# Performance work log

Measured on AMD Instinct MI355X. Metric: run time of the kernel, lower is better.

## Reference

```python
import jax, jax.numpy as jnp
import numpy as np

N_NODES = 50000
N_EDGES = 800000
D_IN = 128
D_HID = 128
D_OUT = 128
N_LAYERS = 2
NEG_SLOPE = 0.2


def leaky(x):
    return jnp.where(x >= 0, x, NEG_SLOPE * x)


def setup_inputs() -> dict:
    key = jax.random.key(0)
    ks = jax.random.split(key, 12)
    s = 1.0 / np.sqrt(D_HID)
    feats = jax.random.normal(ks[0], (N_NODES, D_IN), dtype=jnp.float32)
    src = jax.random.randint(ks[1], (N_EDGES,), 0, N_NODES)
    dst = jax.random.randint(ks[2], (N_EDGES,), 0, N_NODES)
    # SIRConv params per layer: W_Q (dst), W_K (src), W_R (output proj)
    Wq = jax.random.normal(ks[3], (N_LAYERS, D_IN, D_HID), dtype=jnp.float32) * s
    bq = jnp.zeros((N_LAYERS, D_HID), dtype=jnp.float32)
    Wk = jax.random.normal(ks[4], (N_LAYERS, D_IN, D_HID), dtype=jnp.float32) * s
    bk = jnp.zeros((N_LAYERS, D_HID), dtype=jnp.float32)
    Wr = jax.random.normal(ks[5], (N_LAYERS, D_HID, D_HID), dtype=jnp.float32) * s
    br = jnp.zeros((N_LAYERS, D_HID), dtype=jnp.float32)
    # Jumping-knowledge readouts: one per entry of feats_list (input + each layer);
    # input_dim == hidden_dim so weights stack along the leading axis.
    Wro = jax.random.normal(ks[6], (N_LAYERS + 1, D_HID, D_OUT), dtype=jnp.float32) * s
    bro = jnp.zeros((N_LAYERS + 1, D_OUT), dtype=jnp.float32)
    return {"feats": feats, "Wq": Wq, "bq": bq, "Wk": Wk, "bk": bk,
            "Wr": Wr, "br": br, "Wro": Wro, "bro": bro,
            "src": src, "dst": dst}


def reference(feats, Wq, bq, Wk, bk, Wr, br, Wro, bro, src, dst):
    # mean-aggregation denominator: in-degree, clamped to 1
    deg = jax.ops.segment_sum(jnp.ones((N_EDGES,), jnp.float32), dst,
                              num_segments=N_NODES)
    denom = jnp.maximum(deg, 1.0)[:, None]  # [N, 1]

    feats_list = [feats]
    h = feats
    for i in range(N_LAYERS):
        hq = h @ Wq[i] + bq[i]          # [N, H] (dst transform)
        hk = h @ Wk[i] + bk[i]          # [N, H] (src transform)
        m = leaky(hq[dst] + hk[src])    # [E, H] contextualized messages
        agg = jax.ops.segment_sum(m, dst, num_segments=N_NODES) / denom
        h = agg @ Wr[i] + br[i]         # conv output (+ residual = 0)
        h = leaky(h)                    # norm='none', dropout=0
        feats_list.append(h)

    # jumping-knowledge readout: sum of per-stage linear readouts
    score = feats_list[0] @ Wro[0] + bro[0]
    for i in range(1, N_LAYERS + 1):
        score = score + feats_list[i] @ Wro[i] + bro[i]
    return score
```

## Files before the change

### kernel.cpp

```cpp
#include <hip/hip_runtime.h>

#define NN 50000
#define NE 800000
#define D 128
#define NEG 0.2f

#define NBLK1 256
#define TILE1 3125
#define NB2 196
#define CAP2 8192
#define NT64 782

#define SB_PREP 576
#define SB_CONV 6250
#define SB_HIST NBLK1
#define SB_TOTAL (SB_PREP + SB_CONV + SB_HIST)

typedef short bf8_t __attribute__((ext_vector_type(8)));
typedef float f4_t __attribute__((ext_vector_type(4)));

__device__ __forceinline__ unsigned short f2bf(float f) {
  unsigned int u = __float_as_uint(f);
  return (unsigned short)((u + 0x7FFF + ((u >> 16) & 1)) >> 16);
}
__device__ __forceinline__ float bf2f(unsigned int b) { return __uint_as_float(b << 16); }

__device__ __forceinline__ f4_t MF(bf8_t a, bf8_t b, f4_t c) {
  return __builtin_amdgcn_mfma_f32_16x16x32_bf16(a, b, c, 0, 0, 0);
}

__device__ __forceinline__ int swz_u(int u) { return u ^ ((u >> 4) & 7); }


__device__ __forceinline__ void stage_w(unsigned short* wbuf,
                                        const unsigned short* __restrict__ WT, int t) {
#pragma unroll
  for (int i = 0; i < 8; ++i) {
    int u = t + i * 256;
    *(uint4*)(wbuf + swz_u(u) * 8) = *(const uint4*)(WT + u * 8);
  }
}

__device__ __forceinline__ void load_a16(const unsigned short* __restrict__ A,
                                         int base, int l15, int quad, bf8_t (&afr)[4]) {
  int r = base + l15;
  if (r >= NN) r = NN - 1;
  const unsigned short* p = A + (size_t)r * D + quad * 8;
#pragma unroll
  for (int kc = 0; kc < 4; ++kc) afr[kc] = *(const bf8_t*)(p + kc * 32);
}

__device__ __forceinline__ void load_a16_lds(const unsigned short* buf, int wave,
                                             int l15, int quad, bf8_t (&afr)[4]) {
  const int r = wave * 16 + l15;
#pragma unroll
  for (int kc = 0; kc < 4; ++kc)
    afr[kc] = *(const bf8_t*)(buf + swz_u(r * 16 + kc * 4 + quad) * 8);
}

__device__ __forceinline__ void tile16(const unsigned short* wbuf, const bf8_t (&afr)[4],
                                       int l15, int quad, f4_t (&acc)[8]) {
#pragma unroll
  for (int kc = 0; kc < 4; ++kc)
#pragma unroll
    for (int nt = 0; nt < 8; ++nt) {
      bf8_t b = *(const bf8_t*)(wbuf + swz_u((nt * 16 + l15) * 16 + kc * 4 + quad) * 8);
      acc[nt] = MF(afr[kc], b, acc[nt]);
    }
}

__device__ __forceinline__ void store_c(unsigned short* __restrict__ C,
                                        const float* __restrict__ bias,
                                        const f4_t (&acc)[8], int base, int l15, int quad,
                                        bool lk) {
#pragma unroll
  for (int nt = 0; nt < 8; ++nt) {
    int col = nt * 16 + l15;
    float bb = bias[col];
#pragma unroll
    for (int reg = 0; reg < 4; ++reg) {
      int row = base + quad * 4 + reg;
      if (row < NN) {
        float v = acc[nt][reg] + bb;
        if (lk) v = v >= 0.f ? v : NEG * v;
        C[(size_t)row * D + col] = f2bf(v);
      }
    }
  }
}

__global__ __launch_bounds__(256) void setup(
    const float* __restrict__ Wq, const float* __restrict__ Wk,
    const float* __restrict__ Wr, const float* __restrict__ Wro,
    const float* __restrict__ feats, const int* __restrict__ dst,
    unsigned short* __restrict__ WT, unsigned short* __restrict__ x0,
    int* __restrict__ H) {
  __shared__ int cnt[NB2];
  const int b = blockIdx.x;
  const int t = threadIdx.x;
  if (b < SB_PREP) {
    const int m = b >> 6, xb = b & 63;
    const float* src;
    if (m < 2) src = Wq + m * D * D;
    else if (m < 4) src = Wk + (m - 2) * D * D;
    else if (m < 6) src = Wr + (m - 4) * D * D;
    else src = Wro + (m - 6) * D * D;
    const int n = xb * 2 + (t >> 7);
    const int k = t & 127;
    WT[(size_t)m * D * D + n * D + k] = f2bf(src[k * D + n]);
  } else if (b < SB_PREP + SB_CONV) {
    int i = ((b - SB_PREP) * 256 + t) * 4;
    float4 v = *(const float4*)(feats + i);
    ushort4 o = {f2bf(v.x), f2bf(v.y), f2bf(v.z), f2bf(v.w)};
    *(ushort4*)(x0 + i) = o;
  } else {
    const int blk = b - SB_PREP - SB_CONV;
    if (t < NB2) cnt[t] = 0;
    __syncthreads();
    const int beg = blk * TILE1, end = beg + TILE1;
    for (int i = beg + t; i < end; i += 256) atomicAdd(&cnt[dst[i] >> 8], 1);
    __syncthreads();
    if (t < NB2) H[t * NBLK1 + blk] = cnt[t];
  }
}

__global__ __launch_bounds__(256) void p1_scan(const int* __restrict__ H,
                                               int* __restrict__ gofs) {
  __shared__ int sd[256];
  __shared__ int wsum[4];
  const int bin = blockIdx.x;
  const int t = threadIdx.x;
  const int wave = t >> 6, lane = t & 63;
  int part = 0;
  for (int b2 = 0; b2 < bin; ++b2) part += H[b2 * NBLK1 + t];
  for (int off = 32; off; off >>= 1) part += __shfl_down(part, off, 64);
  if (lane == 0) wsum[wave] = part;
  __syncthreads();
  const int base = wsum[0] + wsum[1] + wsum[2] + wsum[3];
  int x = H[bin * NBLK1 + t];
  sd[t] = x;
  __syncthreads();
  int acc = x;
  for (int off = 1; off < 256; off <<= 1) {
    int y = (t >= off) ? sd[t - off] : 0;
    __syncthreads();
    acc += y;
    sd[t] = acc;
    __syncthreads();
  }
  gofs[bin * NBLK1 + t] = base + (acc - x);
}

__global__ __launch_bounds__(256) void p1_scatter(const int* __restrict__ src,
                                                  const int* __restrict__ dst,
                                                  const int* __restrict__ gofs,
                                                  unsigned int* __restrict__ ebuf) {
  __shared__ int lofs[NB2];
  const int t = threadIdx.x;
  const int blk = blockIdx.x;
  if (t < NB2) lofs[t] = gofs[t * NBLK1 + blk];
  __syncthreads();
  const int beg = blk * TILE1, end = beg + TILE1;
  for (int i = beg + t; i < end; i += 256) {
    unsigned int d = (unsigned int)dst[i];
    int pos = atomicAdd(&lofs[d >> 8], 1);
    ebuf[pos] = (unsigned int)src[i] | (d << 16);
  }
}

__global__ __launch_bounds__(256) void sort_qk0(
    const int* __restrict__ gofs, const unsigned int* __restrict__ ebuf,
    int* __restrict__ ssrc, int* __restrict__ rowptr, int* __restrict__ deg,
    const unsigned short* __restrict__ x0,
    const unsigned short* __restrict__ WTq, const float* __restrict__ bq_,
    const unsigned short* __restrict__ WTk, const float* __restrict__ bk_,
    unsigned short* __restrict__ hq, unsigned short* __restrict__ hk) {
  __shared__ __align__(16) unsigned char smraw[35840];
  const int t = threadIdx.x;
  const int gx = blockIdx.x;
  if (gx < NB2) {
    int* cnt = (int*)smraw;
    int* fill = cnt + 256;
    int* sd = fill + 256;
    unsigned int* sorted = (unsigned int*)(sd + 256);
    const int b = gx;
    const int beg = gofs[b * NBLK1];
    const int end = (b + 1 < NB2) ? gofs[(b + 1) * NBLK1] : NE;
    const int n = end - beg;
    cnt[t] = 0;
    __syncthreads();
    for (int i = beg + t; i < end; i += 256)
      atomicAdd(&cnt[(ebuf[i] >> 16) & 255], 1);
    __syncthreads();
    int x = cnt[t];
    sd[t] = x;
    __syncthreads();
    int acc = x;
    for (int off = 1; off < 256; off <<= 1) {
      int y = (t >= off) ? sd[t - off] : 0;
      __syncthreads();
      acc += y;
      sd[t] = acc;
      __syncthreads();
    }
    const int excl = acc - x;
    fill[t] = excl;
    __syncthreads();
    for (int i = beg + t; i < end; i += 256) {
      unsigned int p = ebuf[i];
      int pos = atomicAdd(&fill[(p >> 16) & 255], 1);
      if (pos < CAP2) sorted[pos] = p;
    }
    __syncthreads();
    for (int i = t; i < n; i += 256) ssrc[beg + i] = (int)(sorted[i] & 0xFFFFu);
    const int node = (b << 8) + t;
    if (node < NN) {
      rowptr[node] = beg + excl;
      deg[node] = x;
    }
    if (b == 0 && t == 0) rowptr[NN] = NE;
  } else {
    unsigned short* wbuf = (unsigned short*)smraw;
    const int g = gx - NB2;
    const int sel = g & 1, tile = g >> 1;
    const int wave = t >> 6, lane = t & 63;
    const int l15 = lane & 15, quad = lane >> 4;
    const int base = tile * 64 + wave * 16;
    stage_w(wbuf, sel ? WTk : WTq, t);
    bf8_t afr[4];
    load_a16(x0, base, l15, quad, afr);
    __syncthreads();
    f4_t acc[8] = {};
    tile16(wbuf, afr, l15, quad, acc);
    store_c(sel ? hk : hq, sel ? bk_ : bq_, acc, base, l15, quad, false);
  }
}

#define PROC(kb)                                                     \
  {                                                                  \
    float m;                                                         \
    m = q[0] + bf2f(kb.x & 0xFFFFu); a[0] += m >= 0.f ? m : NEG * m; \
    m = q[1] + bf2f(kb.x >> 16);     a[1] += m >= 0.f ? m : NEG * m; \
    m = q[2] + bf2f(kb.y & 0xFFFFu); a[2] += m >= 0.f ? m : NEG * m; \
    m = q[3] + bf2f(kb.y >> 16);     a[3] += m >= 0.f ? m : NEG * m; \
    m = q[4] + bf2f(kb.z & 0xFFFFu); a[4] += m >= 0.f ? m : NEG * m; \
    m = q[5] + bf2f(kb.z >> 16);     a[5] += m >= 0.f ? m : NEG * m; \
    m = q[6] + bf2f(kb.w & 0xFFFFu); a[6] += m >= 0.f ? m : NEG * m; \
    m = q[7] + bf2f(kb.w >> 16);     a[7] += m >= 0.f ? m : NEG * m; \
  }

__global__ __launch_bounds__(256) void aggregate(
    const int* __restrict__ rowptr, const int* __restrict__ ssrc,
    const int* __restrict__ deg,
    const unsigned short* __restrict__ hq, const unsigned short* __restrict__ hk,
    unsigned short* __restrict__ ag) {
  const int wave = threadIdx.x >> 6, lane = threadIdx.x & 63;
  const int v = blockIdx.x * 4 + wave;
  if (v >= NN) return;
  const int sub = lane & 15, grp = lane >> 4;
  const int beg = rowptr[v], end = rowptr[v + 1];

  uint4 qb = *(const uint4*)(hq + (size_t)v * D + sub * 8);
  float q[8];
  q[0] = bf2f(qb.x & 0xFFFFu); q[1] = bf2f(qb.x >> 16);
  q[2] = bf2f(qb.y & 0xFFFFu); q[3] = bf2f(qb.y >> 16);
  q[4] = bf2f(qb.z & 0xFFFFu); q[5] = bf2f(qb.z >> 16);
  q[6] = bf2f(qb.w & 0xFFFFu); q[7] = bf2f(qb.w >> 16);

  float a[8] = {0.f, 0.f, 0.f, 0.f, 0.f, 0.f, 0.f, 0.f};
  int e = beg + grp;
  for (; e + 12 < end; e += 16) {
    int s0 = ssrc[e];
    int s1 = ssrc[e + 4];
    int s2 = ssrc[e + 8];
    int s3 = ssrc[e + 12];
    uint4 k0 = *(const uint4*)(hk + (size_t)s0 * D + sub * 8);
    uint4 k1 = *(const uint4*)(hk + (size_t)s1 * D + sub * 8);
    uint4 k2 = *(const uint4*)(hk + (size_t)s2 * D + sub * 8);
    uint4 k3 = *(const uint4*)(hk + (size_t)s3 * D + sub * 8);
    PROC(k0);
    PROC(k1);
    PROC(k2);
    PROC(k3);
  }
  for (; e + 4 < end; e += 8) {
    int s0 = ssrc[e];
    int s1 = ssrc[e + 4];
    uint4 k0 = *(const uint4*)(hk + (size_t)s0 * D + sub * 8);
    uint4 k1 = *(const uint4*)(hk + (size_t)s1 * D + sub * 8);
    PROC(k0);
    PROC(k1);
  }
  if (e < end) {
    int s0 = ssrc[e];
    uint4 k0 = *(const uint4*)(hk + (size_t)s0 * D + sub * 8);
    PROC(k0);
  }
#pragma unroll
  for (int j = 0; j < 8; ++j) {
    a[j] += __shfl_xor(a[j], 16, 64);
    a[j] += __shfl_xor(a[j], 32, 64);
  }
  if (grp == 0) {
    float inv = 1.f / fmaxf((float)deg[v], 1.f);
    uint4 o;
    o.x = (unsigned int)f2bf(a[0] * inv) | ((unsigned int)f2bf(a[1] * inv) << 16);
    o.y = (unsigned int)f2bf(a[2] * inv) | ((unsigned int)f2bf(a[3] * inv) << 16);
    o.z = (unsigned int)f2bf(a[4] * inv) | ((unsigned int)f2bf(a[5] * inv) << 16);
    o.w = (unsigned int)f2bf(a[6] * inv) | ((unsigned int)f2bf(a[7] * inv) << 16);
    *(uint4*)(ag + (size_t)v * D + sub * 8) = o;
  }
}

__global__ __launch_bounds__(256) void wr_qk1(
    const unsigned short* __restrict__ ag,
    const unsigned short* __restrict__ WTr, const float* __restrict__ brr,
    unsigned short* __restrict__ h1,
    const unsigned short* __restrict__ WTq, const float* __restrict__ bq1,
    unsigned short* __restrict__ hq,
    const unsigned short* __restrict__ WTk, const float* __restrict__ bk1,
    unsigned short* __restrict__ hk) {
  __shared__ unsigned short wbuf[D * D];
  __shared__ unsigned short abuf[64 * D];
  const int t = threadIdx.x, wave = t >> 6, lane = t & 63;
  const int l15 = lane & 15, quad = lane >> 4;
  const int tb = blockIdx.x * 64;
  const int base = tb + wave * 16;

  stage_w(wbuf, WTr, t);
  bf8_t afr[4];
  load_a16(ag, base, l15, quad, afr);
  __syncthreads();
  f4_t acc[8] = {};
  tile16(wbuf, afr, l15, quad, acc);
#pragma unroll
  for (int nt = 0; nt < 8; ++nt) {
    int col = nt * 16 + l15;
    float bb = brr[col];
#pragma unroll
    for (int reg = 0; reg < 4; ++reg) {
      int rl = wave * 16 + quad * 4 + reg;
      float v = acc[nt][reg] + bb;
      v = v >= 0.f ? v : NEG * v;
      int s = rl * D + col;
      abuf[s ^ ((rl & 7) << 3)] = f2bf(v);
    }
  }
  __syncthreads();

#pragma unroll
  for (int i = 0; i < 4; ++i) {
    int u = t + i * 256;
    int row = tb + (u >> 4);
    if (row < NN)
      *(uint4*)(h1 + (size_t)tb * D + u * 8) = *(const uint4*)(abuf + swz_u(u) * 8);
  }
  bf8_t hfr[4];
  load_a16_lds(abuf, wave, l15, quad, hfr);

  stage_w(wbuf, WTq, t);
  __syncthreads();
  f4_t accq[8] = {};
  tile16(wbuf, hfr, l15, quad, accq);
  store_c(hq, bq1, accq, base, l15, quad, false);
  __syncthreads();

  stage_w(wbuf, WTk, t);
  __syncthreads();
  f4_t acck[8] = {};
  tile16(wbuf, hfr, l15, quad, acck);
  store_c(hk, bk1, acck, base, l15, quad, false);
}

__global__ __launch_bounds__(256) void wr_ro(
    const unsigned short* __restrict__ ag,
    const unsigned short* __restrict__ WTr, const float* __restrict__ brr,
    const unsigned short* __restrict__ x0,
    const unsigned short* __restrict__ h1,
    const unsigned short* __restrict__ WTro, const float* __restrict__ bro_,
    float* __restrict__ out) {
  __shared__ unsigned short wbuf[D * D];
  __shared__ unsigned short abuf[64 * D];
  const int t = threadIdx.x, wave = t >> 6, lane = t & 63;
  const int l15 = lane & 15, quad = lane >> 4;
  const int tb = blockIdx.x * 64;
  const int base = tb + wave * 16;

  stage_w(wbuf, WTr, t);
  bf8_t afr[4];
  load_a16(ag, base, l15, quad, afr);
  __syncthreads();
  f4_t acch[8] = {};
  tile16(wbuf, afr, l15, quad, acch);
#pragma unroll
  for (int nt = 0; nt < 8; ++nt) {
    int col = nt * 16 + l15;
    float bb = brr[col];
#pragma unroll
    for (int reg = 0; reg < 4; ++reg) {
      int rl = wave * 16 + quad * 4 + reg;
      float v = acch[nt][reg] + bb;
      v = v >= 0.f ? v : NEG * v;
      int s = rl * D + col;
      abuf[s ^ ((rl & 7) << 3)] = f2bf(v);
    }
  }
  __syncthreads();

  bf8_t hfr[4];
  load_a16_lds(abuf, wave, l15, quad, hfr);
  f4_t acc[8] = {};

  stage_w(wbuf, WTro + 2 * (size_t)D * D, t);
  __syncthreads();
  tile16(wbuf, hfr, l15, quad, acc);
  __syncthreads();

  stage_w(wbuf, WTro, t);
  load_a16(x0, base, l15, quad, afr);
  __syncthreads();
  tile16(wbuf, afr, l15, quad, acc);
  __syncthreads();

  stage_w(wbuf, WTro + (size_t)D * D, t);
  load_a16(h1, base, l15, quad, afr);
  __syncthreads();
  tile16(wbuf, afr, l15, quad, acc);

#pragma unroll
  for (int nt = 0; nt < 8; ++nt) {
    int col = nt * 16 + l15;
    float bsum = bro_[col] + bro_[D + col] + bro_[2 * D + col];
#pragma unroll
    for (int reg = 0; reg < 4; ++reg) {
      int row = base + quad * 4 + reg;
      if (row < NN) out[(size_t)row * D + col] = acc[nt][reg] + bsum;
    }
  }
}

extern "C" void kernel_launch(void* const* d_in, const int* in_sizes, int n_in,
                              void* d_out, int out_size, void* d_ws, size_t ws_size,
                              hipStream_t stream) {
  const float* feats = (const float*)d_in[0];
  const float* Wq = (const float*)d_in[1];
  const float* bq = (const float*)d_in[2];
  const float* Wk = (const float*)d_in[3];
  const float* bk = (const float*)d_in[4];
  const float* Wr = (const float*)d_in[5];
  const float* br = (const float*)d_in[6];
  const float* Wro = (const float*)d_in[7];
  const float* bro = (const float*)d_in[8];
  const int* src = (const int*)d_in[9];
  const int* dst = (const int*)d_in[10];
  float* out = (float*)d_out;

  size_t off = 0;
  char* base = (char*)d_ws;
  auto alloc = [&](size_t bytes) -> void* {
    void* p = base + off;
    off += (bytes + 255) & ~(size_t)255;
    return p;
  };
  int* H = (int*)alloc((size_t)NB2 * NBLK1 * 4);
  int* gofs = (int*)alloc((size_t)NB2 * NBLK1 * 4);
  unsigned int* ebuf = (unsigned int*)alloc((size_t)NE * 4);
  int* ssrc = (int*)alloc((size_t)NE * 4);
  int* rowptr = (int*)alloc((size_t)(NN + 1) * 4);
  int* deg = (int*)alloc((size_t)NN * 4);
  unsigned short* WT = (unsigned short*)alloc((size_t)9 * D * D * 2);
  unsigned short* x0 = (unsigned short*)alloc((size_t)NN * D * 2);
  unsigned short* hq = (unsigned short*)alloc((size_t)NN * D * 2);
  unsigned short* hk = (unsigned short*)alloc((size_t)NN * D * 2);
  unsigned short* ag = (unsigned short*)alloc((size_t)NN * D * 2);
  unsigned short* h1 = (unsigned short*)alloc((size_t)NN * D * 2);

  const size_t WM = (size_t)D * D;
  const int ab = (NN + 3) / 4;

  setup<<<SB_TOTAL, 256, 0, stream>>>(Wq, Wk, Wr, Wro, feats, dst, WT, x0, H);
  p1_scan<<<NB2, 256, 0, stream>>>(H, gofs);
  p1_scatter<<<NBLK1, 256, 0, stream>>>(src, dst, gofs, ebuf);
  sort_qk0<<<NB2 + 2 * NT64, 256, 0, stream>>>(gofs, ebuf, ssrc, rowptr, deg,
                                               x0, WT + 0 * WM, bq, WT + 2 * WM, bk,
                                               hq, hk);
  aggregate<<<ab, 256, 0, stream>>>(rowptr, ssrc, deg, hq, hk, ag);
  wr_qk1<<<NT64, 256, 0, stream>>>(ag, WT + 4 * WM, br, h1,
                                   WT + 1 * WM, bq + D, hq,
                                   WT + 3 * WM, bk + D, hk);
  aggregate<<<ab, 256, 0, stream>>>(rowptr, ssrc, deg, hq, hk, ag);
  wr_ro<<<NT64, 256, 0, stream>>>(ag, WT + 5 * WM, br + D, x0, h1,
                                  WT + 6 * WM, bro, out);
}
```

Measured before the change: 284.6 us.

## Fuse edge aggregation into the per-tile Wr/Q/K GEMM kernels

The separate aggregate kernels are folded into the following dense-transform kernels. Each 64-row block now aggregates its own nodes into shared memory, then runs the Wr projection and the next Q/K or readout GEMMs on them, so the bf16 aggregate buffer never goes through global memory and two launches disappear. To fit the extra LDS and keep occupancy, weights are staged in 64-column halves, at the cost of more barriers. The layer-1 Q/K outputs go to new hq2/hk2 buffers to avoid read/write races, and the first Q/K GEMM now computes both projections per block from a single feature load. Aggregation moves from 4 nodes per block across 12500 blocks to 16 nodes per wave across 782 blocks, which reduces parallelism for the latency-bound gather.

```diff
diff --git a/kernel.cpp b/kernel.cpp
--- a/kernel.cpp
+++ b/kernel.cpp
@@ -32,12 +32,12 @@
 __device__ __forceinline__ int swz_u(int u) { return u ^ ((u >> 4) & 7); }
 
 
-__device__ __forceinline__ void stage_w(unsigned short* wbuf,
-                                        const unsigned short* __restrict__ WT, int t) {
-#pragma unroll
-  for (int i = 0; i < 8; ++i) {
+__device__ __forceinline__ void stage_wh(unsigned short* wbuf,
+                                         const unsigned short* __restrict__ WTh, int t) {
+#pragma unroll
+  for (int i = 0; i < 4; ++i) {
     int u = t + i * 256;
-    *(uint4*)(wbuf + swz_u(u) * 8) = *(const uint4*)(WT + u * 8);
+    *(uint4*)(wbuf + swz_u(u) * 8) = *(const uint4*)(WTh + u * 8);
   }
 }
 
@@ -58,30 +58,30 @@
     afr[kc] = *(const bf8_t*)(buf + swz_u(r * 16 + kc * 4 + quad) * 8);
 }
 
-__device__ __forceinline__ void tile16(const unsigned short* wbuf, const bf8_t (&afr)[4],
-                                       int l15, int quad, f4_t (&acc)[8]) {
+__device__ __forceinline__ void tile16h(const unsigned short* wbuf, const bf8_t (&afr)[4],
+                                        int l15, int quad, f4_t* acc4) {
 #pragma unroll
   for (int kc = 0; kc < 4; ++kc)
 #pragma unroll
-    for (int nt = 0; nt < 8; ++nt) {
+    for (int nt = 0; nt < 4; ++nt) {
       bf8_t b = *(const bf8_t*)(wbuf + swz_u((nt * 16 + l15) * 16 + kc * 4 + quad) * 8);
-      acc[nt] = MF(afr[kc], b, acc[nt]);
-    }
-}
-
-__device__ __forceinline__ void store_c(unsigned short* __restrict__ C,
-                                        const float* __restrict__ bias,
-                                        const f4_t (&acc)[8], int base, int l15, int quad,
-                                        bool lk) {
-#pragma unroll
-  for (int nt = 0; nt < 8; ++nt) {
-    int col = nt * 16 + l15;
+      acc4[nt] = MF(afr[kc], b, acc4[nt]);
+    }
+}
+
+__device__ __forceinline__ void store_c8(unsigned short* __restrict__ C,
+                                         const float* __restrict__ bias,
+                                         const f4_t (&acc)[8], int base, int l15,
+                                         int quad, bool lk) {
+#pragma unroll
+  for (int j = 0; j < 8; ++j) {
+    int col = (j >> 2) * 64 + (j & 3) * 16 + l15;
     float bb = bias[col];
 #pragma unroll
     for (int reg = 0; reg < 4; ++reg) {
       int row = base + quad * 4 + reg;
       if (row < NN) {
-        float v = acc[nt][reg] + bb;
+        float v = acc[j][reg] + bb;
         if (lk) v = v >= 0.f ? v : NEG * v;
         C[(size_t)row * D + col] = f2bf(v);
       }
@@ -221,18 +221,31 @@
     if (b == 0 && t == 0) rowptr[NN] = NE;
   } else {
     unsigned short* wbuf = (unsigned short*)smraw;
-    const int g = gx - NB2;
-    const int sel = g & 1, tile = g >> 1;
+    const int tile = gx - NB2;
     const int wave = t >> 6, lane = t & 63;
     const int l15 = lane & 15, quad = lane >> 4;
     const int base = tile * 64 + wave * 16;
-    stage_w(wbuf, sel ? WTk : WTq, t);
     bf8_t afr[4];
     load_a16(x0, base, l15, quad, afr);
-    __syncthreads();
-    f4_t acc[8] = {};
-    tile16(wbuf, afr, l15, quad, acc);
-    store_c(sel ? hk : hq, sel ? bk_ : bq_, acc, base, l15, quad, false);
+    stage_wh(wbuf, WTq, t);
+    __syncthreads();
+    f4_t aq[8] = {};
+    tile16h(wbuf, afr, l15, quad, aq);
+    __syncthreads();
+    stage_wh(wbuf, WTq + 64 * D, t);
+    __syncthreads();
+    tile16h(wbuf, afr, l15, quad, aq + 4);
+    store_c8(hq, bq_, aq, base, l15, quad, false);
+    __syncthreads();
+    stage_wh(wbuf, WTk, t);
+    __syncthreads();
+    f4_t ak[8] = {};
+    tile16h(wbuf, afr, l15, quad, ak);
+    __syncthreads();
+    stage_wh(wbuf, WTk + 64 * D, t);
+    __syncthreads();
+    tile16h(wbuf, afr, l15, quad, ak + 4);
+    store_c8(hk, bk_, ak, base, l15, quad, false);
   }
 }
 
@@ -249,24 +262,26 @@
     m = q[7] + bf2f(kb.w >> 16);     a[7] += m >= 0.f ? m : NEG * m; \
   }
 
-__global__ __launch_bounds__(256) void aggregate(
+__device__ __forceinline__ void agg_node(
+    int v, int rl, int sub, int grp,
     const int* __restrict__ rowptr, const int* __restrict__ ssrc,
     const int* __restrict__ deg,
     const unsigned short* __restrict__ hq, const unsigned short* __restrict__ hk,
-    unsigned short* __restrict__ ag) {
-  const int wave = threadIdx.x >> 6, lane = threadIdx.x & 63;
-  const int v = blockIdx.x * 4 + wave;
-  if (v >= NN) return;
-  const int sub = lane & 15, grp = lane >> 4;
+    unsigned short* abuf) {
+  if (v >= NN) {
+    if (grp == 0) {
+      uint4 z = {0u, 0u, 0u, 0u};
+      *(uint4*)(abuf + swz_u(rl * 16 + sub) * 8) = z;
+    }
+    return;
+  }
   const int beg = rowptr[v], end = rowptr[v + 1];
-
   uint4 qb = *(const uint4*)(hq + (size_t)v * D + sub * 8);
   float q[8];
   q[0] = bf2f(qb.x & 0xFFFFu); q[1] = bf2f(qb.x >> 16);
   q[2] = bf2f(qb.y & 0xFFFFu); q[3] = bf2f(qb.y >> 16);
   q[4] = bf2f(qb.z & 0xFFFFu); q[5] = bf2f(qb.z >> 16);
   q[6] = bf2f(qb.w & 0xFFFFu); q[7] = bf2f(qb.w >> 16);
-
   float a[8] = {0.f, 0.f, 0.f, 0.f, 0.f, 0.f, 0.f, 0.f};
   int e = beg + grp;
   for (; e + 12 < end; e += 16) {
@@ -308,46 +323,63 @@
     o.y = (unsigned int)f2bf(a[2] * inv) | ((unsigned int)f2bf(a[3] * inv) << 16);
     o.z = (unsigned int)f2bf(a[4] * inv) | ((unsigned int)f2bf(a[5] * inv) << 16);
     o.w = (unsigned int)f2bf(a[6] * inv) | ((unsigned int)f2bf(a[7] * inv) << 16);
-    *(uint4*)(ag + (size_t)v * D + sub * 8) = o;
-  }
-}
-
-__global__ __launch_bounds__(256) void wr_qk1(
-    const unsigned short* __restrict__ ag,
+    *(uint4*)(abuf + swz_u(rl * 16 + sub) * 8) = o;
+  }
+}
+
+#define ACC_TO_ABUF(ACC, BIAS)                                        \
+  {                                                                   \
+    _Pragma("unroll") for (int j = 0; j < 8; ++j) {                   \
+      int col = (j >> 2) * 64 + (j & 3) * 16 + l15;                   \
+      float bb = (BIAS)[col];                                         \
+      _Pragma("unroll") for (int reg = 0; reg < 4; ++reg) {           \
+        int rl = wave * 16 + quad * 4 + reg;                          \
+        float v = ACC[j][reg] + bb;                                   \
+        v = v >= 0.f ? v : NEG * v;                                   \
+        int s = rl * D + col;                                         \
+        abuf[s ^ ((rl & 7) << 3)] = f2bf(v);                          \
+      }                                                               \
+    }                                                                 \
+  }
+
+__global__ __launch_bounds__(256) void agg_wr_qk1(
+    const int* __restrict__ rowptr, const int* __restrict__ ssrc,
+    const int* __restrict__ deg,
+    const unsigned short* __restrict__ hq, const unsigned short* __restrict__ hk,
     const unsigned short* __restrict__ WTr, const float* __restrict__ brr,
     unsigned short* __restrict__ h1,
     const unsigned short* __restrict__ WTq, const float* __restrict__ bq1,
-    unsigned short* __restrict__ hq,
+    unsigned short* __restrict__ hq2,
     const unsigned short* __restrict__ WTk, const float* __restrict__ bk1,
-    unsigned short* __restrict__ hk) {
-  __shared__ unsigned short wbuf[D * D];
+    unsigned short* __restrict__ hk2) {
+  __shared__ unsigned short wbuf[64 * D];
   __shared__ unsigned short abuf[64 * D];
   const int t = threadIdx.x, wave = t >> 6, lane = t & 63;
   const int l15 = lane & 15, quad = lane >> 4;
+  const int sub = lane & 15, grp = lane >> 4;
   const int tb = blockIdx.x * 64;
   const int base = tb + wave * 16;
 
-  stage_w(wbuf, WTr, t);
-  bf8_t afr[4];
-  load_a16(ag, base, l15, quad, afr);
-  __syncthreads();
+  stage_wh(wbuf, WTr, t);
+  for (int n = 0; n < 16; ++n)
+    agg_node(base + n, wave * 16 + n, sub, grp, rowptr, ssrc, deg, hq, hk, abuf);
+  __syncthreads();
+
+  bf8_t gfr[4];
+  load_a16_lds(abuf, wave, l15, quad, gfr);
   f4_t acc[8] = {};
-  tile16(wbuf, afr, l15, quad, acc);
-#pragma unroll
-  for (int nt = 0; nt < 8; ++nt) {
-    int col = nt * 16 + l15;
-    float bb = brr[col];
-#pragma unroll
-    for (int reg = 0; reg < 4; ++reg) {
-      int rl = wave * 16 + quad * 4 + reg;
-      float v = acc[nt][reg] + bb;
-      v = v >= 0.f ? v : NEG * v;
-      int s = rl * D + col;
-      abuf[s ^ ((rl & 7) << 3)] = f2bf(v);
-    }
-  }
-  __syncthreads();
-
+  tile16h(wbuf, gfr, l15, quad, acc);
+  __syncthreads();
+  stage_wh(wbuf, WTr + 64 * D, t);
+  __syncthreads();
+  tile16h(wbuf, gfr, l15, quad, acc + 4);
+  __syncthreads();
+
+  ACC_TO_ABUF(acc, brr);
+  __syncthreads();
+
+  bf8_t hfr[4];
+  load_a16_lds(abuf, wave, l15, quad, hfr);
 #pragma unroll
   for (int i = 0; i < 4; ++i) {
     int u = t + i * 256;
@@ -355,86 +387,106 @@
     if (row < NN)
       *(uint4*)(h1 + (size_t)tb * D + u * 8) = *(const uint4*)(abuf + swz_u(u) * 8);
   }
-  bf8_t hfr[4];
-  load_a16_lds(abuf, wave, l15, quad, hfr);
-
-  stage_w(wbuf, WTq, t);
-  __syncthreads();
-  f4_t accq[8] = {};
-  tile16(wbuf, hfr, l15, quad, accq);
-  store_c(hq, bq1, accq, base, l15, quad, false);
-  __syncthreads();
-
-  stage_w(wbuf, WTk, t);
-  __syncthreads();
-  f4_t acck[8] = {};
-  tile16(wbuf, hfr, l15, quad, acck);
-  store_c(hk, bk1, acck, base, l15, quad, false);
-}
-
-__global__ __launch_bounds__(256) void wr_ro(
-    const unsigned short* __restrict__ ag,
+
+  stage_wh(wbuf, WTq, t);
+  __syncthreads();
+  f4_t aq[8] = {};
+  tile16h(wbuf, hfr, l15, quad, aq);
+  __syncthreads();
+  stage_wh(wbuf, WTq + 64 * D, t);
+  __syncthreads();
+  tile16h(wbuf, hfr, l15, quad, aq + 4);
+  store_c8(hq2, bq1, aq, base, l15, quad, false);
+  __syncthreads();
+
+  stage_wh(wbuf, WTk, t);
+  __syncthreads();
+  f4_t ak[8] = {};
+  tile16h(wbuf, hfr, l15, quad, ak);
+  __syncthreads();
+  stage_wh(wbuf, WTk + 64 * D, t);
+  __syncthreads();
+  tile16h(wbuf, hfr, l15, quad, ak + 4);
+  store_c8(hk2, bk1, ak, base, l15, quad, false);
+}
+
+__global__ __launch_bounds__(256) void agg_wr_ro(
+    const int* __restrict__ rowptr, const int* __restrict__ ssrc,
+    const int* __restrict__ deg,
+    const unsigned short* __restrict__ hq2, const unsigned short* __restrict__ hk2,
     const unsigned short* __restrict__ WTr, const float* __restrict__ brr,
     const unsigned short* __restrict__ x0,
     const unsigned short* __restrict__ h1,
     const unsigned short* __restrict__ WTro, const float* __restrict__ bro_,
     float* __restrict__ out) {
-  __shared__ unsigned short wbuf[D * D];
+  __shared__ unsigned short wbuf[64 * D];
   __shared__ unsigned short abuf[64 * D];
   const int t = threadIdx.x, wave = t >> 6, lane = t & 63;
   const int l15 = lane & 15, quad = lane >> 4;
+  const int sub = lane & 15, grp = lane >> 4;
   const int tb = blockIdx.x * 64;
   const int base = tb + wave * 16;
-
-  stage_w(wbuf, WTr, t);
-  bf8_t afr[4];
-  load_a16(ag, base, l15, quad, afr);
-  __syncthreads();
+  const size_t WM = (size_t)D * D;
+
+  stage_wh(wbuf, WTr, t);
+  for (int n = 0; n < 16; ++n)
+    agg_node(base + n, wave * 16 + n, sub, grp, rowptr, ssrc, deg, hq2, hk2, abuf);
+  __syncthreads();
+
+  bf8_t gfr[4];
+  load_a16_lds(abuf, wave, l15, quad, gfr);
   f4_t acch[8] = {};
-  tile16(wbuf, afr, l15, quad, acch);
-#pragma unroll
-  for (int nt = 0; nt < 8; ++nt) {
-    int col = nt * 16 + l15;
-    float bb = brr[col];
-#pragma unroll
-    for (int reg = 0; reg < 4; ++reg) {
-      int rl = wave * 16 + quad * 4 + reg;
-      float v = acch[nt][reg] + bb;
-      v = v >= 0.f ? v : NEG * v;
-      int s = rl * D + col;
-      abuf[s ^ ((rl & 7) << 3)] = f2bf(v);
-    }
-  }
+  tile16h(wbuf, gfr, l15, quad, acch);
+  __syncthreads();
+  stage_wh(wbuf, WTr + 64 * D, t);
+  __syncthreads();
+  tile16h(wbuf, gfr, l15, quad, acch + 4);
+  __syncthreads();
+
+  ACC_TO_ABUF(acch, brr);
   __syncthreads();
 
   bf8_t hfr[4];
   load_a16_lds(abuf, wave, l15, quad, hfr);
   f4_t acc[8] = {};
 
-  stage_w(wbuf, WTro + 2 * (size_t)D * D, t);
-  __syncthreads();
-  tile16(wbuf, hfr, l15, quad, acc);
-  __syncthreads();
-
-  stage_w(wbuf, WTro, t);
+  stage_wh(wbuf, WTro + 2 * WM, t);
+  __syncthreads();
+  tile16h(wbuf, hfr, l15, quad, acc);
+  __syncthreads();
+  stage_wh(wbuf, WTro + 2 * WM + 64 * D, t);
+  __syncthreads();
+  tile16h(wbuf, hfr, l15, quad, acc + 4);
+  __syncthreads();
+
+  bf8_t afr[4];
   load_a16(x0, base, l15, quad, afr);
-  __syncthreads();
-  tile16(wbuf, afr, l15, quad, acc);
-  __syncthreads();
-
-  stage_w(wbuf, WTro + (size_t)D * D, t);
+  stage_wh(wbuf, WTro, t);
+  __syncthreads();
+  tile16h(wbuf, afr, l15, quad, acc);
+  __syncthreads();
+  stage_wh(wbuf, WTro + 64 * D, t);
+  __syncthreads();
+  tile16h(wbuf, afr, l15, quad, acc + 4);
+  __syncthreads();
+
   load_a16(h1, base, l15, quad, afr);
-  __syncthreads();
-  tile16(wbuf, afr, l15, quad, acc);
-
-#pragma unroll
-  for (int nt = 0; nt < 8; ++nt) {
-    int col = nt * 16 + l15;
+  stage_wh(wbuf, WTro + WM, t);
+  __syncthreads();
+  tile16h(wbuf, afr, l15, quad, acc);
+  __syncthreads();
+  stage_wh(wbuf, WTro + WM + 64 * D, t);
+  __syncthreads();
+  tile16h(wbuf, afr, l15, quad, acc + 4);
+
+#pragma unroll
+  for (int j = 0; j < 8; ++j) {
+    int col = (j >> 2) * 64 + (j & 3) * 16 + l15;
     float bsum = bro_[col] + bro_[D + col] + bro_[2 * D + col];
 #pragma unroll
     for (int reg = 0; reg < 4; ++reg) {
       int row = base + quad * 4 + reg;
-      if (row < NN) out[(size_t)row * D + col] = acc[nt][reg] + bsum;
+      if (row < NN) out[(size_t)row * D + col] = acc[j][reg] + bsum;
     }
   }
 }
@@ -472,23 +524,23 @@
   unsigned short* x0 = (unsigned short*)alloc((size_t)NN * D * 2);
   unsigned short* hq = (unsigned short*)alloc((size_t)NN * D * 2);
   unsigned short* hk = (unsigned short*)alloc((size_t)NN * D * 2);
-  unsigned short* ag = (unsigned short*)alloc((size_t)NN * D * 2);
+  unsigned short* hq2 = (unsigned short*)alloc((size_t)NN * D * 2);
+  unsigned short* hk2 = (unsigned short*)alloc((size_t)NN * D * 2);
   unsigned short* h1 = (unsigned short*)alloc((size_t)NN * D * 2);
 
   const size_t WM = (size_t)D * D;
-  const int ab = (NN + 3) / 4;
 
   setup<<<SB_TOTAL, 256, 0, stream>>>(Wq, Wk, Wr, Wro, feats, dst, WT, x0, H);
   p1_scan<<<NB2, 256, 0, stream>>>(H, gofs);
   p1_scatter<<<NBLK1, 256, 0, stream>>>(src, dst, gofs, ebuf);
-  sort_qk0<<<NB2 + 2 * NT64, 256, 0, stream>>>(gofs, ebuf, ssrc, rowptr, deg,
-                                               x0, WT + 0 * WM, bq, WT + 2 * WM, bk,
-                                               hq, hk);
-  aggregate<<<ab, 256, 0, stream>>>(rowptr, ssrc, deg, hq, hk, ag);
-  wr_qk1<<<NT64, 256, 0, stream>>>(ag, WT + 4 * WM, br, h1,
-                                   WT + 1 * WM, bq + D, hq,
-                                   WT + 3 * WM, bk + D, hk);
-  aggregate<<<ab, 256, 0, stream>>>(rowptr, ssrc, deg, hq, hk, ag);
-  wr_ro<<<NT64, 256, 0, stream>>>(ag, WT + 5 * WM, br + D, x0, h1,
-                                  WT + 6 * WM, bro, out);
-}
+  sort_qk0<<<NB2 + NT64, 256, 0, stream>>>(gofs, ebuf, ssrc, rowptr, deg,
+                                           x0, WT + 0 * WM, bq, WT + 2 * WM, bk,
+                                           hq, hk);
+  agg_wr_qk1<<<NT64, 256, 0, stream>>>(rowptr, ssrc, deg, hq, hk,
+                                       WT + 4 * WM, br, h1,
+                                       WT + 1 * WM, bq + D, hq2,
+                                       WT + 3 * WM, bk + D, hk2);
+  agg_wr_ro<<<NT64, 256, 0, stream>>>(rowptr, ssrc, deg, hq2, hk2,
+                                      WT + 5 * WM, br + D, x0, h1,
+                                      WT + 6 * WM, bro, out);
+}
```

Measured after the change: 372.8 us. 31.0% more time.
